# Performance work log

Hardware: AMD Instinct MI355X
Metric: run time of the kernel (lower is better)

The kernel has to match this reference:

```python
import jax, jax.numpy as jnp
import numpy as np

N_NODES = 100000
N_EDGES = 1600000
IN_F = 64
HID = 64
OUT_F = 64


def _param(key, shape, fan_in):
    return jax.random.normal(key, shape, dtype=jnp.float32) * (1.0 / np.sqrt(fan_in))


def setup_inputs() -> dict:
    key = jax.random.key(0)
    ks = jax.random.split(key, 12)
    features = jax.random.normal(ks[0], (N_NODES, IN_F), dtype=jnp.float32)
    src = jax.random.randint(ks[1], (N_EDGES,), 0, N_NODES, dtype=jnp.int32)
    dst = jax.random.randint(ks[2], (N_EDGES,), 0, N_NODES, dtype=jnp.int32)
    dims = [(IN_F, HID), (HID, HID), (HID, OUT_F)]
    inp = {"features": features, "src": src, "dst": dst}
    for i, (din, dout) in enumerate(dims):
        inp[f"W_self{i}"] = _param(ks[3 + 3 * i], (din, dout), din)
        inp[f"W_neigh{i}"] = _param(ks[4 + 3 * i], (din, dout), din)
        inp[f"b{i}"] = jnp.zeros((dout,), dtype=jnp.float32)
    return inp


def _sage_layer(h, src, dst, W_self, W_neigh, b, deg_inv, n_nodes, act):
    # mean aggregation over in-neighbors: gather src feats, segment-sum into dst
    msum = jax.ops.segment_sum(h[src], dst, num_segments=n_nodes)  # [N, d]
    h_neigh = msum * deg_inv  # mean (zero-degree nodes -> 0, matching DGL)
    out = h @ W_self + h_neigh @ W_neigh + b
    return jax.nn.relu(out) if act else out


def reference(features, src, dst, W_self0, W_neigh0, b0, W_self1, W_neigh1, b1, W_self2, W_neigh2, b2):
    n = features.shape[0]
    deg = jax.ops.segment_sum(jnp.ones((src.shape[0],), jnp.float32), dst, num_segments=n)
    deg_inv = (1.0 / jnp.maximum(deg, 1.0))[:, None]  # [N, 1]
    h = _sage_layer(features, src, dst, W_self0, W_neigh0, b0, deg_inv, n, act=True)
    h = _sage_layer(h, src, dst, W_self1, W_neigh1, b1, deg_inv, n, act=True)
    h = _sage_layer(h, src, dst, W_self2, W_neigh2, b2, deg_inv, n, act=False)
    return h
```

## Files before the change

kernel.cpp:

```cpp
#include <hip/hip_runtime.h>

#define NF 64
#define BUCKET 128
#define MAXB 8192
#define EPB 4096

typedef __attribute__((ext_vector_type(8))) short bf16x8;
typedef __attribute__((ext_vector_type(4))) float f32x4;
typedef __attribute__((ext_vector_type(4))) unsigned int u32x4;

__device__ __forceinline__ float bf2f(unsigned short x) {
    union { unsigned int u; float f; } v; v.u = ((unsigned int)x) << 16; return v.f;
}
__device__ __forceinline__ unsigned short f2bf(float x) {
    union { float f; unsigned int u; } v; v.f = x;
    unsigned int r = (v.u + 0x7FFFu + ((v.u >> 16) & 1u)) >> 16;
    return (unsigned short)r;
}


__global__ __launch_bounds__(256) void bhist_kernel(const int* __restrict__ dst,
                                                    int* __restrict__ bins,
                                                    int n_edges, int nb) {
    __shared__ int h[MAXB];
    for (int i = threadIdx.x; i < nb; i += 256) h[i] = 0;
    __syncthreads();
    int base = blockIdx.x * EPB;
    int lim = min(base + EPB, n_edges);
    for (int i = base + threadIdx.x; i < lim; i += 256)
        atomicAdd(&h[dst[i] >> 7], 1);
    __syncthreads();
    for (int i = threadIdx.x; i < nb; i += 256) {
        int v = h[i];
        if (v) atomicAdd(&bins[i], v);
    }
}

__global__ __launch_bounds__(1024) void bscan_kernel(const int* __restrict__ bins,
                                                     int* __restrict__ bptr,
                                                     int* __restrict__ gcur, int nb) {
    __shared__ int sd[1024];
    int carry = 0;
    if (threadIdx.x == 0) bptr[0] = 0;
    for (int base = 0; base < nb; base += 1024) {
        int i = base + threadIdx.x;
        int v = (i < nb) ? bins[i] : 0;
        sd[threadIdx.x] = v;
        __syncthreads();
        for (int off = 1; off < 1024; off <<= 1) {
            int t = (threadIdx.x >= off) ? sd[threadIdx.x - off] : 0;
            __syncthreads();
            sd[threadIdx.x] += t;
            __syncthreads();
        }
        if (i < nb) {
            int ex = carry + sd[threadIdx.x] - v;
            bptr[i + 1] = carry + sd[threadIdx.x];
            gcur[i] = ex;
        }
        int last = sd[1023];
        __syncthreads();
        carry += last;
    }
}

__global__ __launch_bounds__(256) void bscatter_kernel(const int* __restrict__ src,
                                                       const int* __restrict__ dst,
                                                       int* __restrict__ gcur,
                                                       unsigned* __restrict__ bedges,
                                                       int n_edges, int nb) {
    __shared__ int h[MAXB];
    for (int i = threadIdx.x; i < nb; i += 256) h[i] = 0;
    __syncthreads();
    int base = blockIdx.x * EPB;
    int myDst[16], mySrc[16];
#pragma unroll
    for (int k = 0; k < 16; ++k) {
        int i = base + k * 256 + threadIdx.x;
        if (i < n_edges) {
            myDst[k] = dst[i];
            mySrc[k] = src[i];
            atomicAdd(&h[myDst[k] >> 7], 1);
        } else {
            myDst[k] = -1;
        }
    }
    __syncthreads();
    for (int i = threadIdx.x; i < nb; i += 256) {
        int v = h[i];
        h[i] = v ? atomicAdd(&gcur[i], v) : 0;
    }
    __syncthreads();
#pragma unroll
    for (int k = 0; k < 16; ++k) {
        if (myDst[k] >= 0) {
            int bin = myDst[k] >> 7;
            int pos = atomicAdd(&h[bin], 1);
            bedges[pos] = ((unsigned)mySrc[k] << 7) | (unsigned)(myDst[k] & 127);
        }
    }
}

__global__ __launch_bounds__(256) void bfinal_kernel(
    const unsigned* __restrict__ bedges, const int* __restrict__ bptr,
    int* __restrict__ row_ptr, int* __restrict__ col,
    int n_nodes, int n_edges, int nb) {
    __shared__ int cnt[BUCKET];
    __shared__ int sa[BUCKET], sb2[BUCKET];
    int tid = threadIdx.x;
    int b = blockIdx.x;
    int beg = bptr[b], end = bptr[b + 1];
    if (tid < BUCKET) cnt[tid] = 0;
    __syncthreads();
    for (int i = beg + tid; i < end; i += 256)
        atomicAdd(&cnt[bedges[i] & (BUCKET - 1)], 1);
    __syncthreads();
    if (tid < BUCKET) sa[tid] = cnt[tid];
    __syncthreads();
    int* pin = sa; int* pout = sb2;
    for (int off = 1; off < BUCKET; off <<= 1) {
        if (tid < BUCKET) pout[tid] = pin[tid] + ((tid >= off) ? pin[tid - off] : 0);
        __syncthreads();
        int* t = pin; pin = pout; pout = t;
    }
    int nodeBase = b * BUCKET;
    if (tid < BUCKET && nodeBase + tid < n_nodes)
        row_ptr[nodeBase + tid] = beg + (tid ? pin[tid - 1] : 0);
    if (b == nb - 1 && tid == 0) row_ptr[n_nodes] = n_edges;
    __syncthreads();
    if (tid < BUCKET) cnt[tid] = 0;
    __syncthreads();
    for (int i = beg + tid; i < end; i += 256) {
        unsigned e = bedges[i];
        int d = e & (BUCKET - 1);
        int pos = beg + (d ? pin[d - 1] : 0) + atomicAdd(&cnt[d], 1);
        col[pos] = (int)(e >> 7);
    }
}


__global__ void convert_kernel(const float* __restrict__ in, unsigned short* __restrict__ X, int n_nodes) {
    int t = blockIdx.x * blockDim.x + threadIdx.x;
    int total = n_nodes * 16;
    if (t >= total) return;
    int n = t >> 4, g = t & 15;
    float4 v = *reinterpret_cast<const float4*>(in + (size_t)n * 64 + g * 4);
    ushort4 o;
    o.x = f2bf(v.x); o.y = f2bf(v.y); o.z = f2bf(v.z); o.w = f2bf(v.w);
    *reinterpret_cast<ushort4*>(X + (size_t)n * 128 + g * 4) = o;
}

__global__ void wtrans_kernel(const float* __restrict__ Ws0, const float* __restrict__ Wn0,
                              const float* __restrict__ Ws1, const float* __restrict__ Wn1,
                              const float* __restrict__ Ws2, const float* __restrict__ Wn2,
                              unsigned short* __restrict__ WT) {
    int t = blockIdx.x * blockDim.x + threadIdx.x;
    if (t >= 3 * 64 * 128) return;
    int layer = t >> 13;
    int r = t & 8191;
    int j = r >> 7, k = r & 127;
    const float* Ws = layer == 0 ? Ws0 : (layer == 1 ? Ws1 : Ws2);
    const float* Wn = layer == 0 ? Wn0 : (layer == 1 ? Wn1 : Wn2);
    float v = (k < 64) ? Ws[k * 64 + j] : Wn[(k - 64) * 64 + j];
    WT[t] = f2bf(v);
}

__global__ __launch_bounds__(256) void aggregate_bf16_kernel(
    unsigned short* __restrict__ X, const int* __restrict__ row_ptr, const int* __restrict__ col,
    int n_nodes) {
    int lane = threadIdx.x & 63;
    int wid = threadIdx.x >> 6;
    int q = lane >> 3;
    int j = lane & 7;
    int n = blockIdx.x * 4 + wid;
    if (n >= n_nodes) return;
    int beg = row_ptr[n], end = row_ptr[n + 1];
    float a[8] = {0.f, 0.f, 0.f, 0.f, 0.f, 0.f, 0.f, 0.f};
    for (int i = beg; i < end; i += 16) {
        int e0 = i + q, e1 = i + 8 + q;
        bool ok0 = e0 < end, ok1 = e1 < end;
        int s0 = col[ok0 ? e0 : end - 1];
        int s1 = col[ok1 ? e1 : end - 1];
        u32x4 v0 = *reinterpret_cast<const u32x4*>(X + (size_t)s0 * 128 + j * 8);
        u32x4 v1 = *reinterpret_cast<const u32x4*>(X + (size_t)s1 * 128 + j * 8);
        if (ok0) {
#pragma unroll
            for (int k = 0; k < 4; ++k) {
                union { unsigned u; float f; } lo, hi;
                lo.u = v0[k] << 16; hi.u = v0[k] & 0xffff0000u;
                a[2 * k] += lo.f; a[2 * k + 1] += hi.f;
            }
        }
        if (ok1) {
#pragma unroll
            for (int k = 0; k < 4; ++k) {
                union { unsigned u; float f; } lo, hi;
                lo.u = v1[k] << 16; hi.u = v1[k] & 0xffff0000u;
                a[2 * k] += lo.f; a[2 * k + 1] += hi.f;
            }
        }
    }
#pragma unroll
    for (int k = 0; k < 8; ++k) {
        a[k] += __shfl_xor(a[k], 8);
        a[k] += __shfl_xor(a[k], 16);
        a[k] += __shfl_xor(a[k], 32);
    }
    if (q == 0) {
        float dinv = 1.0f / fmaxf((float)(end - beg), 1.0f);
        u32x4 o;
#pragma unroll
        for (int k = 0; k < 4; ++k)
            o[k] = ((unsigned)f2bf(a[2 * k + 1] * dinv) << 16) | f2bf(a[2 * k] * dinv);
        *reinterpret_cast<u32x4*>(X + (size_t)n * 128 + 64 + j * 8) = o;
    }
}

__global__ __launch_bounds__(256) void linear_mfma_kernel(
    const unsigned short* __restrict__ X, const unsigned short* __restrict__ WT,
    const float* __restrict__ bias, unsigned short* __restrict__ outBf,
    float* __restrict__ outF32, int n_nodes, int do_relu) {
    int lane = threadIdx.x & 63;
    int wid = threadIdx.x >> 6;
    int l15 = lane & 15;
    int lg = lane >> 4;

    bf16x8 wf[4][4];
#pragma unroll
    for (int ft = 0; ft < 4; ++ft)
#pragma unroll
        for (int ks = 0; ks < 4; ++ks)
            wf[ft][ks] = *reinterpret_cast<const bf16x8*>(
                WT + (size_t)(ft * 16 + l15) * 128 + ks * 32 + lg * 8);

    float4 bv[4];
#pragma unroll
    for (int ft = 0; ft < 4; ++ft)
        bv[ft] = *reinterpret_cast<const float4*>(bias + ft * 16 + lg * 4);

    int tiles = (n_nodes + 15) >> 4;
    for (int tile = blockIdx.x * 4 + wid; tile < tiles; tile += gridDim.x * 4) {
        int nodeBase = tile * 16;
        int nrow = nodeBase + l15;
        int rrow = nrow < n_nodes ? nrow : n_nodes - 1;

        bf16x8 xf[4];
#pragma unroll
        for (int ks = 0; ks < 4; ++ks)
            xf[ks] = *reinterpret_cast<const bf16x8*>(X + (size_t)rrow * 128 + ks * 32 + lg * 8);

        f32x4 acc[4];
#pragma unroll
        for (int ft = 0; ft < 4; ++ft) acc[ft] = (f32x4){0.f, 0.f, 0.f, 0.f};
#pragma unroll
        for (int ks = 0; ks < 4; ++ks) {
#pragma unroll
            for (int ft = 0; ft < 4; ++ft)
                acc[ft] = __builtin_amdgcn_mfma_f32_16x16x32_bf16(wf[ft][ks], xf[ks], acc[ft], 0, 0, 0);
        }

        if (nrow < n_nodes) {
#pragma unroll
            for (int ft = 0; ft < 4; ++ft) {
                float4 v;
                v.x = acc[ft][0] + bv[ft].x;
                v.y = acc[ft][1] + bv[ft].y;
                v.z = acc[ft][2] + bv[ft].z;
                v.w = acc[ft][3] + bv[ft].w;
                if (do_relu) {
                    v.x = fmaxf(v.x, 0.f); v.y = fmaxf(v.y, 0.f);
                    v.z = fmaxf(v.z, 0.f); v.w = fmaxf(v.w, 0.f);
                }
                int fbase = ft * 16 + lg * 4;
                if (outF32) {
                    *reinterpret_cast<float4*>(outF32 + (size_t)nrow * 64 + fbase) = v;
                } else {
                    ushort4 o;
                    o.x = f2bf(v.x); o.y = f2bf(v.y); o.z = f2bf(v.z); o.w = f2bf(v.w);
                    *reinterpret_cast<ushort4*>(outBf + (size_t)nrow * 128 + fbase) = o;
                }
            }
        }
    }
}


__global__ void deg_kernel(const int* __restrict__ dst, float* __restrict__ deg, int n_edges) {
    int e = blockIdx.x * blockDim.x + threadIdx.x;
    if (e < n_edges) unsafeAtomicAdd(&deg[dst[e]], 1.0f);
}

__global__ void inv_kernel(float* __restrict__ deg, int n) {
    int i = blockIdx.x * blockDim.x + threadIdx.x;
    if (i < n) deg[i] = 1.0f / fmaxf(deg[i], 1.0f);
}

__global__ __launch_bounds__(256) void scatter_kernel(
    const float* __restrict__ h, const int* __restrict__ src, const int* __restrict__ dst,
    float* __restrict__ agg, int n_edges) {
    int t = blockIdx.x * blockDim.x + threadIdx.x;
    int e = t >> 4;
    if (e >= n_edges) return;
    int q = (t & 15) * 4;
    int s = src[e];
    int d = dst[e];
    float4 v = *reinterpret_cast<const float4*>(h + (size_t)s * NF + q);
    float* o = agg + (size_t)d * NF + q;
    unsafeAtomicAdd(o + 0, v.x);
    unsafeAtomicAdd(o + 1, v.y);
    unsafeAtomicAdd(o + 2, v.z);
    unsafeAtomicAdd(o + 3, v.w);
}

__global__ __launch_bounds__(256) void linear_kernel(
    const float* __restrict__ h, const float* __restrict__ agg, const float* __restrict__ deginv,
    const float* __restrict__ Ws, const float* __restrict__ Wn, const float* __restrict__ bias,
    float* __restrict__ out, int n_nodes, int do_relu) {
    __shared__ float sWs[NF * NF];
    __shared__ float sWn[NF * NF];
    __shared__ float sb[NF];
    for (int i = threadIdx.x; i < NF * NF; i += 256) {
        sWs[i] = Ws[i];
        sWn[i] = Wn[i];
    }
    if (threadIdx.x < NF) sb[threadIdx.x] = bias[threadIdx.x];
    __syncthreads();
    int j = threadIdx.x & 63;
    int sub = threadIdx.x >> 6;
    for (int n = blockIdx.x * 4 + sub; n < n_nodes; n += gridDim.x * 4) {
        const float4* hr = reinterpret_cast<const float4*>(h + (size_t)n * NF);
        const float4* ar = reinterpret_cast<const float4*>(agg + (size_t)n * NF);
        float accS = 0.f, accN = 0.f;
#pragma unroll
        for (int k4 = 0; k4 < 16; ++k4) {
            float4 hv = hr[k4];
            float4 av = ar[k4];
            int kb = k4 * 4;
            accS += hv.x * sWs[(kb + 0) * NF + j];
            accN += av.x * sWn[(kb + 0) * NF + j];
            accS += hv.y * sWs[(kb + 1) * NF + j];
            accN += av.y * sWn[(kb + 1) * NF + j];
            accS += hv.z * sWs[(kb + 2) * NF + j];
            accN += av.z * sWn[(kb + 2) * NF + j];
            accS += hv.w * sWs[(kb + 3) * NF + j];
            accN += av.w * sWn[(kb + 3) * NF + j];
        }
        float val = accS + deginv[n] * accN + sb[j];
        if (do_relu) val = fmaxf(val, 0.f);
        out[(size_t)n * NF + j] = val;
    }
}


extern "C" void kernel_launch(void* const* d_in, const int* in_sizes, int n_in,
                              void* d_out, int out_size, void* d_ws, size_t ws_size,
                              hipStream_t stream) {
    const float* features = (const float*)d_in[0];
    const int* src = (const int*)d_in[1];
    const int* dst = (const int*)d_in[2];
    const float* Ws0 = (const float*)d_in[3];
    const float* Wn0 = (const float*)d_in[4];
    const float* b0  = (const float*)d_in[5];
    const float* Ws1 = (const float*)d_in[6];
    const float* Wn1 = (const float*)d_in[7];
    const float* b1  = (const float*)d_in[8];
    const float* Ws2 = (const float*)d_in[9];
    const float* Wn2 = (const float*)d_in[10];
    const float* b2  = (const float*)d_in[11];

    const int n_nodes = in_sizes[0] / NF;
    const int n_edges = in_sizes[1];
    float* out = (float*)d_out;

    const int nb = (n_nodes + BUCKET - 1) / BUCKET;
    const size_t alignNB = (((size_t)nb + 1) * 4 + 255) / 256 * 256;
    const size_t alignN = (((size_t)n_nodes + 64) * 4 + 255) / 256 * 256;
    const size_t alignE = ((size_t)n_edges * 4 + 255) / 256 * 256;
    const size_t xBytes = ((size_t)n_nodes * 128 * 2 + 255) / 256 * 256;
    const size_t wtBytes = 3 * 64 * 128 * 2;

    dim3 blk(256);
    const int nEB = (n_edges + EPB - 1) / EPB;
    const int waveBlocks = (n_nodes + 3) / 4;
    const int tiles = (n_nodes + 15) / 16;
    const int linBlocks = (tiles + 3) / 4;

    const size_t need = 3 * alignNB + alignN + alignE + 2 * xBytes + wtBytes;
    const bool outFits = (size_t)out_size * sizeof(float) >= (size_t)n_edges * sizeof(unsigned);

    if (ws_size >= need && nb <= MAXB && n_nodes < (1 << 25) && outFits) {
        char* ws = (char*)d_ws;
        int* bins     = (int*)ws;
        int* bptr     = (int*)(ws + alignNB);
        int* gcur     = (int*)(ws + 2 * alignNB);
        int* row_ptr  = (int*)(ws + 3 * alignNB);
        int* col      = (int*)(ws + 3 * alignNB + alignN);
        unsigned short* X0  = (unsigned short*)(ws + 3 * alignNB + alignN + alignE);
        unsigned short* X1  = (unsigned short*)((char*)X0 + xBytes);
        unsigned short* WT  = (unsigned short*)((char*)X1 + xBytes);
        unsigned short* WT0 = WT;
        unsigned short* WT1 = WT + 64 * 128;
        unsigned short* WT2 = WT + 2 * 64 * 128;
        unsigned* bedges = (unsigned*)d_out;

        hipMemsetAsync(bins, 0, (size_t)nb * sizeof(int), stream);
        bhist_kernel<<<nEB, blk, 0, stream>>>(dst, bins, n_edges, nb);
        bscan_kernel<<<1, 1024, 0, stream>>>(bins, bptr, gcur, nb);
        bscatter_kernel<<<nEB, blk, 0, stream>>>(src, dst, gcur, bedges, n_edges, nb);
        bfinal_kernel<<<nb, blk, 0, stream>>>(bedges, bptr, row_ptr, col, n_nodes, n_edges, nb);

        convert_kernel<<<(n_nodes * 16 + 255) / 256, blk, 0, stream>>>(features, X0, n_nodes);
        wtrans_kernel<<<96, blk, 0, stream>>>(Ws0, Wn0, Ws1, Wn1, Ws2, Wn2, WT);

        aggregate_bf16_kernel<<<waveBlocks, blk, 0, stream>>>(X0, row_ptr, col, n_nodes);
        linear_mfma_kernel<<<linBlocks, blk, 0, stream>>>(X0, WT0, b0, X1, nullptr, n_nodes, 1);
        aggregate_bf16_kernel<<<waveBlocks, blk, 0, stream>>>(X1, row_ptr, col, n_nodes);
        linear_mfma_kernel<<<linBlocks, blk, 0, stream>>>(X1, WT1, b1, X0, nullptr, n_nodes, 1);
        aggregate_bf16_kernel<<<waveBlocks, blk, 0, stream>>>(X0, row_ptr, col, n_nodes);
        linear_mfma_kernel<<<linBlocks, blk, 0, stream>>>(X0, WT2, b2, nullptr, out, n_nodes, 0);
    } else {
        char* ws = (char*)d_ws;
        size_t degBytes = (((size_t)n_nodes * 4) + 255) / 256 * 256;
        float* deg = (float*)ws;
        float* agg = (float*)(ws + degBytes);
        float* h1  = agg + (size_t)n_nodes * NF;
        int scatBlocks = (n_edges * 16 + 255) / 256;
        int eBlocks = (n_edges + 255) / 256;
        size_t rowBytes = (size_t)n_nodes * NF * sizeof(float);

        hipMemsetAsync(deg, 0, (size_t)n_nodes * sizeof(float), stream);
        deg_kernel<<<eBlocks, blk, 0, stream>>>(dst, deg, n_edges);
        inv_kernel<<<(n_nodes + 255) / 256, blk, 0, stream>>>(deg, n_nodes);

        hipMemsetAsync(agg, 0, rowBytes, stream);
        scatter_kernel<<<scatBlocks, blk, 0, stream>>>(features, src, dst, agg, n_edges);
        linear_kernel<<<waveBlocks, blk, 0, stream>>>(features, agg, deg, Ws0, Wn0, b0, out, n_nodes, 1);

        hipMemsetAsync(agg, 0, rowBytes, stream);
        scatter_kernel<<<scatBlocks, blk, 0, stream>>>(out, src, dst, agg, n_edges);
        linear_kernel<<<waveBlocks, blk, 0, stream>>>(out, agg, deg, Ws1, Wn1, b1, h1, n_nodes, 1);

        hipMemsetAsync(agg, 0, rowBytes, stream);
        scatter_kernel<<<scatBlocks, blk, 0, stream>>>(h1, src, dst, agg, n_edges);
        linear_kernel<<<waveBlocks, blk, 0, stream>>>(h1, agg, deg, Ws2, Wn2, b2, out, n_nodes, 0);
    }
}
```

Baseline: 258.7 us.

## Enlarge edge chunks, merge convert and weight-transpose kernels, add nontemporal loads

Edges per block in the histogram and scatter kernels go from 4096 to 16384, giving fewer blocks and fewer global atomics on the bucket counters. The scatter kernel now rereads dst and src from memory on a second pass instead of holding them in registers. The feature-conversion and weight-transpose kernels are merged into one launch, and nontemporal loads are used for dst in the histogram and for col in aggregation. With 1.6M edges the larger chunks leave only about 98 blocks, which may underfill the GPU and lengthen each block's serial loop.

```diff
diff --git a/kernel.cpp b/kernel.cpp
--- a/kernel.cpp
+++ b/kernel.cpp
@@ -3,7 +3,7 @@
 #define NF 64
 #define BUCKET 128
 #define MAXB 8192
-#define EPB 4096
+#define CEPB 16384
 
 typedef __attribute__((ext_vector_type(8))) short bf16x8;
 typedef __attribute__((ext_vector_type(4))) float f32x4;
@@ -25,10 +25,10 @@
     __shared__ int h[MAXB];
     for (int i = threadIdx.x; i < nb; i += 256) h[i] = 0;
     __syncthreads();
-    int base = blockIdx.x * EPB;
-    int lim = min(base + EPB, n_edges);
+    int base = blockIdx.x * CEPB;
+    int lim = min(base + CEPB, n_edges);
     for (int i = base + threadIdx.x; i < lim; i += 256)
-        atomicAdd(&h[dst[i] >> 7], 1);
+        atomicAdd(&h[__builtin_nontemporal_load(dst + i) >> 7], 1);
     __syncthreads();
     for (int i = threadIdx.x; i < nb; i += 256) {
         int v = h[i];
@@ -54,9 +54,8 @@
             __syncthreads();
         }
         if (i < nb) {
-            int ex = carry + sd[threadIdx.x] - v;
             bptr[i + 1] = carry + sd[threadIdx.x];
-            gcur[i] = ex;
+            gcur[i] = carry + sd[threadIdx.x] - v;
         }
         int last = sd[1023];
         __syncthreads();
@@ -72,32 +71,20 @@
     __shared__ int h[MAXB];
     for (int i = threadIdx.x; i < nb; i += 256) h[i] = 0;
     __syncthreads();
-    int base = blockIdx.x * EPB;
-    int myDst[16], mySrc[16];
-#pragma unroll
-    for (int k = 0; k < 16; ++k) {
-        int i = base + k * 256 + threadIdx.x;
-        if (i < n_edges) {
-            myDst[k] = dst[i];
-            mySrc[k] = src[i];
-            atomicAdd(&h[myDst[k] >> 7], 1);
-        } else {
-            myDst[k] = -1;
-        }
-    }
+    int base = blockIdx.x * CEPB;
+    int lim = min(base + CEPB, n_edges);
+    for (int i = base + threadIdx.x; i < lim; i += 256)
+        atomicAdd(&h[dst[i] >> 7], 1);
     __syncthreads();
     for (int i = threadIdx.x; i < nb; i += 256) {
         int v = h[i];
         h[i] = v ? atomicAdd(&gcur[i], v) : 0;
     }
     __syncthreads();
-#pragma unroll
-    for (int k = 0; k < 16; ++k) {
-        if (myDst[k] >= 0) {
-            int bin = myDst[k] >> 7;
-            int pos = atomicAdd(&h[bin], 1);
-            bedges[pos] = ((unsigned)mySrc[k] << 7) | (unsigned)(myDst[k] & 127);
-        }
+    for (int i = base + threadIdx.x; i < lim; i += 256) {
+        int d = dst[i];
+        int pos = atomicAdd(&h[d >> 7], 1);
+        bedges[pos] = ((unsigned)src[i] << 7) | (unsigned)(d & 127);
     }
 }
 
@@ -138,31 +125,31 @@
     }
 }
 
-
-__global__ void convert_kernel(const float* __restrict__ in, unsigned short* __restrict__ X, int n_nodes) {
-    int t = blockIdx.x * blockDim.x + threadIdx.x;
-    int total = n_nodes * 16;
-    if (t >= total) return;
-    int n = t >> 4, g = t & 15;
-    float4 v = *reinterpret_cast<const float4*>(in + (size_t)n * 64 + g * 4);
-    ushort4 o;
-    o.x = f2bf(v.x); o.y = f2bf(v.y); o.z = f2bf(v.z); o.w = f2bf(v.w);
-    *reinterpret_cast<ushort4*>(X + (size_t)n * 128 + g * 4) = o;
-}
-
-__global__ void wtrans_kernel(const float* __restrict__ Ws0, const float* __restrict__ Wn0,
-                              const float* __restrict__ Ws1, const float* __restrict__ Wn1,
-                              const float* __restrict__ Ws2, const float* __restrict__ Wn2,
-                              unsigned short* __restrict__ WT) {
-    int t = blockIdx.x * blockDim.x + threadIdx.x;
-    if (t >= 3 * 64 * 128) return;
-    int layer = t >> 13;
-    int r = t & 8191;
-    int j = r >> 7, k = r & 127;
-    const float* Ws = layer == 0 ? Ws0 : (layer == 1 ? Ws1 : Ws2);
-    const float* Wn = layer == 0 ? Wn0 : (layer == 1 ? Wn1 : Wn2);
-    float v = (k < 64) ? Ws[k * 64 + j] : Wn[(k - 64) * 64 + j];
-    WT[t] = f2bf(v);
+__global__ void stage_kernel(const float* __restrict__ in, unsigned short* __restrict__ X,
+                             const float* __restrict__ Ws0, const float* __restrict__ Wn0,
+                             const float* __restrict__ Ws1, const float* __restrict__ Wn1,
+                             const float* __restrict__ Ws2, const float* __restrict__ Wn2,
+                             unsigned short* __restrict__ WT, int n_nodes, int convBlocks) {
+    if (blockIdx.x < (unsigned)convBlocks) {
+        int t = blockIdx.x * 256 + threadIdx.x;
+        int total = n_nodes * 16;
+        if (t >= total) return;
+        int n = t >> 4, g = t & 15;
+        float4 v = *reinterpret_cast<const float4*>(in + (size_t)n * 64 + g * 4);
+        ushort4 o;
+        o.x = f2bf(v.x); o.y = f2bf(v.y); o.z = f2bf(v.z); o.w = f2bf(v.w);
+        *reinterpret_cast<ushort4*>(X + (size_t)n * 128 + g * 4) = o;
+    } else {
+        int t = (blockIdx.x - convBlocks) * 256 + threadIdx.x;
+        if (t >= 3 * 64 * 128) return;
+        int layer = t >> 13;
+        int r = t & 8191;
+        int j = r >> 7, k = r & 127;
+        const float* Ws = layer == 0 ? Ws0 : (layer == 1 ? Ws1 : Ws2);
+        const float* Wn = layer == 0 ? Wn0 : (layer == 1 ? Wn1 : Wn2);
+        float v = (k < 64) ? Ws[k * 64 + j] : Wn[(k - 64) * 64 + j];
+        WT[t] = f2bf(v);
+    }
 }
 
 __global__ __launch_bounds__(256) void aggregate_bf16_kernel(
@@ -179,8 +166,8 @@
     for (int i = beg; i < end; i += 16) {
         int e0 = i + q, e1 = i + 8 + q;
         bool ok0 = e0 < end, ok1 = e1 < end;
-        int s0 = col[ok0 ? e0 : end - 1];
-        int s1 = col[ok1 ? e1 : end - 1];
+        int s0 = __builtin_nontemporal_load(col + (ok0 ? e0 : end - 1));
+        int s1 = __builtin_nontemporal_load(col + (ok1 ? e1 : end - 1));
         u32x4 v0 = *reinterpret_cast<const u32x4*>(X + (size_t)s0 * 128 + j * 8);
         u32x4 v1 = *reinterpret_cast<const u32x4*>(X + (size_t)s1 * 128 + j * 8);
         if (ok0) {
@@ -380,10 +367,11 @@
     const size_t wtBytes = 3 * 64 * 128 * 2;
 
     dim3 blk(256);
-    const int nEB = (n_edges + EPB - 1) / EPB;
+    const int nCB = (n_edges + CEPB - 1) / CEPB;
     const int waveBlocks = (n_nodes + 3) / 4;
     const int tiles = (n_nodes + 15) / 16;
     const int linBlocks = (tiles + 3) / 4;
+    const int convBlocks = (n_nodes * 16 + 255) / 256;
 
     const size_t need = 3 * alignNB + alignN + alignE + 2 * xBytes + wtBytes;
     const bool outFits = (size_t)out_size * sizeof(float) >= (size_t)n_edges * sizeof(unsigned);
@@ -404,13 +392,13 @@
         unsigned* bedges = (unsigned*)d_out;
 
         hipMemsetAsync(bins, 0, (size_t)nb * sizeof(int), stream);
-        bhist_kernel<<<nEB, blk, 0, stream>>>(dst, bins, n_edges, nb);
+        bhist_kernel<<<nCB, blk, 0, stream>>>(dst, bins, n_edges, nb);
         bscan_kernel<<<1, 1024, 0, stream>>>(bins, bptr, gcur, nb);
-        bscatter_kernel<<<nEB, blk, 0, stream>>>(src, dst, gcur, bedges, n_edges, nb);
+        bscatter_kernel<<<nCB, blk, 0, stream>>>(src, dst, gcur, bedges, n_edges, nb);
         bfinal_kernel<<<nb, blk, 0, stream>>>(bedges, bptr, row_ptr, col, n_nodes, n_edges, nb);
 
-        convert_kernel<<<(n_nodes * 16 + 255) / 256, blk, 0, stream>>>(features, X0, n_nodes);
-        wtrans_kernel<<<96, blk, 0, stream>>>(Ws0, Wn0, Ws1, Wn1, Ws2, Wn2, WT);
+        stage_kernel<<<convBlocks + 96, blk, 0, stream>>>(features, X0,
+            Ws0, Wn0, Ws1, Wn1, Ws2, Wn2, WT, n_nodes, convBlocks);
 
         aggregate_bf16_kernel<<<waveBlocks, blk, 0, stream>>>(X0, row_ptr, col, n_nodes);
         linear_mfma_kernel<<<linBlocks, blk, 0, stream>>>(X0, WT0, b0, X1, nullptr, n_nodes, 1);
```

Result: slower. 318.6 us (+23.2%).
